# Kernel optimization log

Hardware: AMD Instinct MI355X
Metric: run time of the kernel (lower is better)

## Reference

```python
import jax, jax.numpy as jnp
import numpy as np

D = 1024; H = 16; N = 64; F = 4096
B = 1; T = 2048
W_LORA = 64; A_LORA = 64; V_LORA = 32; G_LORA = 128


def rmsnorm(x, w, eps=1e-6):
    x32 = x.astype(jnp.float32)
    var = jnp.mean(x32 * x32, axis=-1, keepdims=True)
    return w * (x32 * jax.lax.rsqrt(var + eps))


def rwkv7_scan(r, w_log, k, v, a, b, state):
    # r,w_log,k,v,a,b: [B,T,H,N]; state: [B,H,N,N] (value dim, key dim)
    decay = jnp.exp(w_log)  # kernel applies exp to the log-decay w = -exp(w_pre)
    def step(S, inp):
        r_t, d_t, k_t, v_t, a_t, b_t = inp  # each [B,H,N]
        sa = jnp.einsum('bhij,bhj->bhi', S, a_t)
        S = S * d_t[:, :, None, :] + sa[..., None] * b_t[:, :, None, :] + v_t[..., None] * k_t[:, :, None, :]
        o_t = jnp.einsum('bhij,bhj->bhi', S, r_t)
        return S, o_t
    seq = tuple(jnp.moveaxis(t, 1, 0) for t in (r, decay, k, v, a, b))  # [T,B,H,N]
    state_f, o = jax.lax.scan(step, state, seq)
    return jnp.moveaxis(o, 0, 1), state_f  # [B,T,H,N], [B,H,N,N]


def setup_inputs() -> dict:
    key = jax.random.key(0)
    ks = iter(jax.random.split(key, 64))
    def nrm(shape, s=1.0):
        return jax.random.normal(next(ks), shape, dtype=jnp.float32) * s
    def uni(shape):
        return jax.random.uniform(next(ks), shape, dtype=jnp.float32)
    WS = 0.02  # weight scale for big matrices
    inp = {
        'x': nrm((B, T, D)),
        'x_prev': nrm((B, D)),
        'v_first': nrm((B, T, D)),
        'state': jnp.zeros((B, H, N, N), jnp.float32),
        'ln1_w': jnp.ones((D,), jnp.float32),
        'ln2_w': jnp.ones((D,), jnp.float32),
        'x_r': uni((1, 1, D)), 'x_w': uni((1, 1, D)), 'x_k': uni((1, 1, D)),
        'x_v': uni((1, 1, D)), 'x_a': uni((1, 1, D)), 'x_g': uni((1, 1, D)),
        'w0': nrm((1, 1, D), 0.5), 'w1': nrm((D, W_LORA), WS), 'w2': nrm((W_LORA, D), WS),
        'a0': nrm((1, 1, D), 0.1), 'a1': nrm((D, A_LORA), WS), 'a2': nrm((A_LORA, D), WS),
        'v0': nrm((1, 1, D), 0.1), 'v1': nrm((D, V_LORA), WS), 'v2': nrm((V_LORA, D), WS),
        'g1': nrm((D, G_LORA), WS), 'g2': nrm((G_LORA, D), WS),
        'k_k': uni((D,)), 'k_a': uni((D,)), 'r_k': nrm((D,), 0.1),
        'R_': nrm((D, D), WS), 'K_': nrm((D, D), WS), 'V_': nrm((D, D), WS), 'O_': nrm((D, D), WS),
        'gate_w': nrm((D, F), WS), 'up_w': nrm((D, F), WS), 'down_w': nrm((F, D), WS),
    }
    return inp


def _block(x, x_prev, v_first, state, ln1_w, ln2_w, x_r, x_w, x_k, x_v, x_a, x_g,
           w0, w1, w2, a0, a1, a2, v0, v1, v2, g1, g2, k_k, k_a, r_k,
           R_, K_, V_, O_, gate_w, up_w, down_w):
    Bx, Tx, _ = x.shape
    xn = rmsnorm(x, ln1_w)  # ln1
    # token shift
    xx = jnp.concatenate([x_prev[:, None, :], xn[:, :-1]], axis=1) - xn
    xr = xn + xx * x_r; xw = xn + xx * x_w; xk = xn + xx * x_k
    xv = xn + xx * x_v; xa = xn + xx * x_a; xg = xn + xx * x_g
    r = xr @ R_
    w_pre = -jax.nn.softplus(-(w0 + jnp.tanh(xw @ w1) @ w2)) - 0.5
    k = xk @ K_
    v = xv @ V_
    a = jax.nn.sigmoid(a0 + (xa @ a1) @ a2)
    g = jax.nn.sigmoid(xg @ g1) @ g2
    kk = (k * k_k).reshape(Bx, Tx, H, N)
    kk = kk / jnp.maximum(jnp.linalg.norm(kk, axis=-1, keepdims=True), 1e-12)
    kk = kk.reshape(Bx, Tx, H * N)
    k = k * (1 + (a - 1) * k_a)
    # layer_id > 0: lerp toward v_first
    v = v + (v_first - v) * jax.nn.sigmoid(v0 + (xv @ v1) @ v2)
    w_log = -jnp.exp(w_pre)  # log-decay passed to the recurrent kernel
    aa = -kk
    bb = kk * a
    hv = lambda t: t.reshape(Bx, Tx, H, N)
    o, state_f = rwkv7_scan(hv(r), hv(w_log), hv(k), hv(v), hv(aa), hv(bb), state)
    o = o.reshape(Bx, Tx, H * N)
    bonus = ((r * k * r_k).reshape(Bx, Tx, H, N).sum(-1, keepdims=True) * v.reshape(Bx, Tx, H, N)).reshape(Bx, Tx, H * N)
    o = o + bonus
    x = x + (o * g) @ O_
    # SwiGLU MLP
    xm = rmsnorm(x, ln2_w)
    x = x + (jax.nn.silu(xm @ gate_w) * (xm @ up_w)) @ down_w
    return x, xn[:, -1], state_f


def reference(x, x_prev, v_first, state, ln1_w, ln2_w, x_r, x_w, x_k, x_v, x_a, x_g,
              w0, w1, w2, a0, a1, a2, v0, v1, v2, g1, g2, k_k, k_a, r_k,
              R_, K_, V_, O_, gate_w, up_w, down_w):
    return _block(x, x_prev, v_first, state, ln1_w, ln2_w, x_r, x_w, x_k, x_v, x_a, x_g,
                  w0, w1, w2, a0, a1, a2, v0, v1, v2, g1, g2, k_k, k_a, r_k,
                  R_, K_, V_, O_, gate_w, up_w, down_w)
```

## Files before the change

kernel.cpp:

```cpp
#include <hip/hip_runtime.h>
#include <math.h>

#define T_ 2048
#define D_ 1024
#define H_ 16
#define N_ 64
#define F_ 4096
#define NCHUNK 32
#define CLEN 64

typedef __attribute__((ext_vector_type(8))) short bf16x8;
typedef __attribute__((ext_vector_type(4))) float f32x4;
typedef __attribute__((address_space(3))) unsigned int lds_u32_t;
typedef __attribute__((address_space(1))) const unsigned int glb_u32_t;

static __device__ __forceinline__ float sigf(float x) { return 1.0f / (1.0f + __expf(-x)); }

static __device__ __forceinline__ ushort f2bf(float f) {
    union { float f; unsigned u; } c; c.f = f;
    unsigned r = (c.u + 0x7FFFu + ((c.u >> 16) & 1u)) >> 16;
    return (ushort)r;
}
static __device__ __forceinline__ float bf2f(ushort h) {
    union { unsigned u; float f; } c; c.u = ((unsigned)h) << 16;
    return c.f;
}

static __device__ __forceinline__ void st4(float* p, float4 v) { *(float4*)p = v; }
static __device__ __forceinline__ void st4(ushort* p, float4 v) {
    ushort4 o; o.x = f2bf(v.x); o.y = f2bf(v.y); o.z = f2bf(v.z); o.w = f2bf(v.w);
    *(ushort4*)p = o;
}

template <typename OutT>
__global__ __launch_bounds__(256) void rmsnorm_kernel(const float* __restrict__ x,
                                                      const float* __restrict__ w,
                                                      OutT* __restrict__ out,
                                                      float* __restrict__ last) {
    const int t = blockIdx.x;
    const int tid = threadIdx.x;
    const float4* xr = (const float4*)(x + (size_t)t * D_);
    float4 v = xr[tid];
    float ss = v.x * v.x + v.y * v.y + v.z * v.z + v.w * v.w;
    ss += __shfl_xor(ss, 1);
    ss += __shfl_xor(ss, 2);
    ss += __shfl_xor(ss, 4);
    ss += __shfl_xor(ss, 8);
    ss += __shfl_xor(ss, 16);
    ss += __shfl_xor(ss, 32);
    __shared__ float red[4];
    if ((tid & 63) == 0) red[tid >> 6] = ss;
    __syncthreads();
    float tot = red[0] + red[1] + red[2] + red[3];
    float scale = rsqrtf(tot * (1.0f / (float)D_) + 1e-6f);
    float4 wv = ((const float4*)w)[tid];
    float4 o;
    o.x = wv.x * v.x * scale;
    o.y = wv.y * v.y * scale;
    o.z = wv.z * v.z * scale;
    o.w = wv.w * v.w * scale;
    st4(out + (size_t)t * D_ + tid * 4, o);
    if (last != nullptr && t == T_ - 1) ((float4*)last)[tid] = o;
}

__global__ __launch_bounds__(256) void shift_kernel(
    const float* __restrict__ xn, const float* __restrict__ x_prev,
    const float* __restrict__ cr, const float* __restrict__ cw, const float* __restrict__ ck,
    const float* __restrict__ cv, const float* __restrict__ ca, const float* __restrict__ cg,
    ushort* __restrict__ xr, ushort* __restrict__ xw, ushort* __restrict__ xk,
    ushort* __restrict__ xv, ushort* __restrict__ xa, ushort* __restrict__ xg) {
    const int i = blockIdx.x * 256 + threadIdx.x;
    const int t = i >> 8, j = i & 255;
    const float4* xn4 = (const float4*)xn;
    float4 cur = xn4[i];
    float4 prev = (t == 0) ? ((const float4*)x_prev)[j] : xn4[i - 256];
    float4 xx;
    xx.x = prev.x - cur.x;
    xx.y = prev.y - cur.y;
    xx.z = prev.z - cur.z;
    xx.w = prev.w - cur.w;
#define APPLY(dst, c)                                   \
    {                                                   \
        float4 cc = ((const float4*)c)[j];              \
        float4 o;                                       \
        o.x = cur.x + xx.x * cc.x;                      \
        o.y = cur.y + xx.y * cc.y;                      \
        o.z = cur.z + xx.z * cc.z;                      \
        o.w = cur.w + xx.w * cc.w;                      \
        st4(dst + (size_t)i * 4, o);                    \
    }
    APPLY(xr, cr)
    APPLY(xw, cw)
    APPLY(xk, ck)
    APPLY(xv, cv)
    APPLY(xa, ca)
    APPLY(xg, cg)
#undef APPLY
}

struct TDesc { const float* in; ushort* out; int K, N, off; };
struct TPack { TDesc d[15]; };

__global__ __launch_bounds__(256) void transpose_cast_multi(TPack p) {
    __shared__ float tile[32][33];
    const int bid = blockIdx.x;
    int di = 0;
#pragma unroll
    for (int i = 1; i < 15; i++)
        if (bid >= p.d[i].off) di = i;
    const TDesc d = p.d[di];
    const int local = bid - d.off;
    const int nt = d.N >> 5;
    const int bx = local % nt, by = local / nt;
    const int tx = threadIdx.x & 31, ty = threadIdx.x >> 5;
    const int n0 = bx * 32, k0 = by * 32;
#pragma unroll
    for (int i = 0; i < 4; i++)
        tile[ty + i * 8][tx] = d.in[(size_t)(k0 + ty + i * 8) * d.N + n0 + tx];
    __syncthreads();
#pragma unroll
    for (int i = 0; i < 4; i++)
        d.out[(size_t)(n0 + ty + i * 8) * d.K + k0 + tx] = f2bf(tile[tx][ty + i * 8]);
}

template <typename OutT, bool ATOMIC>
__global__ __launch_bounds__(256) void mfma_gemm(
    const ushort* __restrict__ A, const ushort* __restrict__ BT, OutT* __restrict__ C,
    const float* __restrict__ res, const float* __restrict__ res2, const float* __restrict__ bias,
    int M, int Ntot, int K, int klen, int epi) {
    __shared__ ushort As[128 * 32];
    __shared__ ushort Bs[128 * 32];
    const int tid = threadIdx.x;
    const int wave = tid >> 6, lane = tid & 63;
    const int wr = wave >> 1, wc = wave & 1;
    const int lrow = lane & 15, quad = lane >> 4;
    const int m0 = blockIdx.y * 128, n0 = blockIdx.x * 128;
    const int kbase = blockIdx.z * klen;
    const int srow = lane >> 2;
    const int scol = (lane & 3) << 3;

    f32x4 acc[4][4] = {};

    for (int k0 = kbase; k0 < kbase + klen; k0 += 32) {
#pragma unroll
        for (int j = 0; j < 2; j++) {
            const int chunk = 2 * wave + j;
            const ushort* ga = A + (size_t)(m0 + chunk * 16 + srow) * K + k0 + scol;
            __builtin_amdgcn_global_load_lds((glb_u32_t*)ga,
                                             (lds_u32_t*)&As[chunk * 512], 16, 0, 0);
            const int brow = n0 + chunk * 16 + srow;
            const ushort* gb = BT + (size_t)brow * K + k0 + scol;
            if (brow < Ntot)
                __builtin_amdgcn_global_load_lds((glb_u32_t*)gb,
                                                 (lds_u32_t*)&Bs[chunk * 512], 16, 0, 0);
        }
        __syncthreads();
        bf16x8 af[4], bfr[4];
#pragma unroll
        for (int mi = 0; mi < 4; mi++)
            af[mi] = *(const bf16x8*)&As[(wr * 64 + mi * 16 + lrow) * 32 + quad * 8];
#pragma unroll
        for (int ni = 0; ni < 4; ni++)
            bfr[ni] = *(const bf16x8*)&Bs[(wc * 64 + ni * 16 + lrow) * 32 + quad * 8];
#pragma unroll
        for (int mi = 0; mi < 4; mi++)
#pragma unroll
            for (int ni = 0; ni < 4; ni++)
                acc[mi][ni] = __builtin_amdgcn_mfma_f32_16x16x32_bf16(af[mi], bfr[ni], acc[mi][ni], 0, 0, 0);
        __syncthreads();
    }

#pragma unroll
    for (int mi = 0; mi < 4; mi++) {
#pragma unroll
        for (int r = 0; r < 4; r++) {
            const int row = m0 + wr * 64 + mi * 16 + quad * 4 + r;
#pragma unroll
            for (int ni = 0; ni < 4; ni++) {
                const int col = n0 + wc * 64 + ni * 16 + lrow;
                if (col < Ntot) {
                    const size_t idx = (size_t)row * Ntot + col;
                    float val = acc[mi][ni][r];
                    if constexpr (ATOMIC) {
                        atomicAdd((float*)&C[idx], val);
                    } else {
                        switch (epi) {
                            case 1: val += res[idx]; break;
                            case 2: val = val * sigf(val); break;
                            default: break;
                        }
                        if constexpr (sizeof(OutT) == 2) C[idx] = (OutT)f2bf(val);
                        else C[idx] = (OutT)val;
                    }
                }
            }
        }
    }
}

struct MMDesc {
    const ushort* A; const ushort* BT;
    float* Cf; ushort* Cb;
    const float* res; const float* res2; const float* bias;
    int Ntot, K, kbase, klen, epi, atomic;
};
template <int NZ>
struct MMPack { MMDesc d[NZ]; };

template <int NZ>
__global__ __launch_bounds__(256) void mfma_gemm_multi(MMPack<NZ> p) {
    const MMDesc d = p.d[blockIdx.z];
    const int n0 = blockIdx.x * 128;
    if (n0 >= d.Ntot) return;
    __shared__ ushort As[128 * 32];
    __shared__ ushort Bs[128 * 32];
    const int tid = threadIdx.x;
    const int wave = tid >> 6, lane = tid & 63;
    const int wr = wave >> 1, wc = wave & 1;
    const int lrow = lane & 15, quad = lane >> 4;
    const int m0 = blockIdx.y * 128;
    const int srow = lane >> 2;
    const int scol = (lane & 3) << 3;
    const int K = d.K, Ntot = d.Ntot;

    f32x4 acc[4][4] = {};

    for (int k0 = d.kbase; k0 < d.kbase + d.klen; k0 += 32) {
#pragma unroll
        for (int j = 0; j < 2; j++) {
            const int chunk = 2 * wave + j;
            const ushort* ga = d.A + (size_t)(m0 + chunk * 16 + srow) * K + k0 + scol;
            __builtin_amdgcn_global_load_lds((glb_u32_t*)ga,
                                             (lds_u32_t*)&As[chunk * 512], 16, 0, 0);
            const int brow = n0 + chunk * 16 + srow;
            const ushort* gb = d.BT + (size_t)brow * K + k0 + scol;
            if (brow < Ntot)
                __builtin_amdgcn_global_load_lds((glb_u32_t*)gb,
                                                 (lds_u32_t*)&Bs[chunk * 512], 16, 0, 0);
        }
        __syncthreads();
        bf16x8 af[4], bfr[4];
#pragma unroll
        for (int mi = 0; mi < 4; mi++)
            af[mi] = *(const bf16x8*)&As[(wr * 64 + mi * 16 + lrow) * 32 + quad * 8];
#pragma unroll
        for (int ni = 0; ni < 4; ni++)
            bfr[ni] = *(const bf16x8*)&Bs[(wc * 64 + ni * 16 + lrow) * 32 + quad * 8];
#pragma unroll
        for (int mi = 0; mi < 4; mi++)
#pragma unroll
            for (int ni = 0; ni < 4; ni++)
                acc[mi][ni] = __builtin_amdgcn_mfma_f32_16x16x32_bf16(af[mi], bfr[ni], acc[mi][ni], 0, 0, 0);
        __syncthreads();
    }

#pragma unroll
    for (int mi = 0; mi < 4; mi++) {
#pragma unroll
        for (int r = 0; r < 4; r++) {
            const int row = m0 + wr * 64 + mi * 16 + quad * 4 + r;
#pragma unroll
            for (int ni = 0; ni < 4; ni++) {
                const int col = n0 + wc * 64 + ni * 16 + lrow;
                if (col < Ntot) {
                    const size_t idx = (size_t)row * Ntot + col;
                    float val = acc[mi][ni][r];
                    if (d.atomic) {
                        atomicAdd(d.Cf + idx, val);
                    } else {
                        switch (d.epi) {
                            case 3: val = tanhf(val); break;
                            case 4: val = sigf(val); break;
                            case 5: val = sigf(d.bias[col] + val); break;
                            case 6: val = __expf(-0.60653065971263342f * sigf(d.bias[col] + val)); break;
                            case 7: {
                                float vr = d.res[idx];
                                val = vr + (d.res2[idx] - vr) * sigf(d.bias[col] + val);
                            } break;
                            default: break;
                        }
                        if (d.Cb) d.Cb[idx] = f2bf(val);
                        else d.Cf[idx] = val;
                    }
                }
            }
        }
    }
}

__global__ __launch_bounds__(256) void kk_kernel(float* __restrict__ k,
                                                 const float* __restrict__ a_sig,
                                                 const float* __restrict__ k_k,
                                                 const float* __restrict__ k_a,
                                                 float* __restrict__ kk,
                                                 float* __restrict__ mb) {
    const int b = blockIdx.x * 4 + (threadIdx.x >> 6);
    const int t = b >> 4, h = b & 15;
    const int lane = threadIdx.x & 63;
    const size_t idx = (size_t)t * D_ + h * N_ + lane;
    const int wi = h * N_ + lane;
    const float kraw = k[idx];
    const float kv = kraw * k_k[wi];
    float ss = kv * kv;
    ss += __shfl_xor(ss, 1);
    ss += __shfl_xor(ss, 2);
    ss += __shfl_xor(ss, 4);
    ss += __shfl_xor(ss, 8);
    ss += __shfl_xor(ss, 16);
    ss += __shfl_xor(ss, 32);
    const float nrm = fmaxf(sqrtf(ss), 1e-12f);
    const float kkn = kv / nrm;
    kk[idx] = kkn;
    mb[idx] = -kkn * a_sig[idx];
    k[idx] = kraw * (1.0f + (a_sig[idx] - 1.0f) * k_a[wi]);
}

#define FOR16(M) M(0) M(1) M(2) M(3) M(4) M(5) M(6) M(7) \
                 M(8) M(9) M(10) M(11) M(12) M(13) M(14) M(15)

__global__ __launch_bounds__(64, 1) void scan_pass1(
    const float* __restrict__ gR, const float* __restrict__ gD, const float* __restrict__ gK,
    const float* __restrict__ gV, const float* __restrict__ gKK, const float* __restrict__ gMB,
    float* __restrict__ Pbuf, float* __restrict__ Lbuf,
    float* __restrict__ zbuf, float* __restrict__ olbuf) {
    const int bid = blockIdx.x;
    const bool isp = bid >= NCHUNK * H_;
    const int sub = isp ? bid - NCHUNK * H_ : bid;
    const int h = sub & 15;
    const int c = sub >> 4;
    const int lane = threadIdx.x;
    const int hb = h * N_;
    const int t0 = c * CLEN;
    const int tend = t0 + CLEN - 1;

    __shared__ __align__(16) unsigned char ring[2 * 2048];

    const int rsel = lane >> 4;
    const int sub4 = (lane & 15) << 2;
    const float* p1 = (rsel == 0 ? gR : rsel == 1 ? gD : rsel == 2 ? gK : gKK)
                      + (size_t)t0 * D_ + hb + sub4;
    const float* p2 = (rsel == 1 ? gV : gMB) + (size_t)t0 * D_ + hb + sub4;

    const float fid = isp ? 1.0f : 0.0f;
#define DECL(q) f32x4 s##q = {(lane == 4 * q + 0) ? fid : 0.0f, \
                              (lane == 4 * q + 1) ? fid : 0.0f, \
                              (lane == 4 * q + 2) ? fid : 0.0f, \
                              (lane == 4 * q + 3) ? fid : 0.0f};
    FOR16(DECL)
#undef DECL

    float* __restrict__ dotOut = isp ? zbuf : olbuf;

    float4 r0a, r0b, r1a, r1b, r2a, r2b, r3a, r3b;

#define LOADQ(qa, qb, tt) {                                                  \
        const size_t _adv = (size_t)((tt) - t0) * D_;                        \
        qa = *(const float4*)(p1 + _adv);                                    \
        qb = *(const float4*)(p2 + _adv); }
#define WRITEQ(sl, qa, qb) {                                                 \
        *(float4*)(ring + (sl) * 2048 + lane * 16) = qa;                     \
        *(float4*)(ring + (sl) * 2048 + 1024 + lane * 16) = qb; }
#define PA(q) { const f32x4 kk4 = sKKr[q]; sacc += s##q * kk4; }
#define PB(q) {                                                   \
        const f32x4 d4 = sDr[q];                                  \
        const f32x4 k4 = sKr[q];                                  \
        const f32x4 m4 = sMBr[q];                                 \
        const f32x4 r4 = sRr[q];                                  \
        s##q = s##q * d4 + (m4 * sap + k4 * vv);                  \
        oacc += s##q * r4;                                        \
    }
#define COMPUTE(sl, tt) {                                                    \
        const unsigned char* sb = (const unsigned char*)ring + (sl) * 2048;  \
        const f32x4* sRr = (const f32x4*)(sb);                               \
        const f32x4* sDr = (const f32x4*)(sb + 256);                         \
        const f32x4* sKr = (const f32x4*)(sb + 512);                         \
        const f32x4* sKKr = (const f32x4*)(sb + 768);                        \
        const f32x4* sMBr = (const f32x4*)(sb + 1024);                       \
        const float* sVr = (const float*)(sb + 1280);                        \
        f32x4 sacc = {0.f, 0.f, 0.f, 0.f};                                   \
        FOR16(PA)                                                            \
        const float sap = (sacc.x + sacc.y) + (sacc.z + sacc.w);             \
        const float vv = isp ? 0.0f : sVr[lane];                             \
        f32x4 oacc = {0.f, 0.f, 0.f, 0.f};                                   \
        FOR16(PB)                                                            \
        dotOut[(size_t)(tt) * D_ + hb + lane] =                              \
            (oacc.x + oacc.y) + (oacc.z + oacc.w); }

    LOADQ(r0a, r0b, t0)
    LOADQ(r1a, r1b, t0 + 1)
    LOADQ(r2a, r2b, t0 + 2)
    LOADQ(r3a, r3b, t0 + 3)
    WRITEQ(0, r0a, r0b)

    for (int t = t0; t < t0 + CLEN; t += 4) {
        WRITEQ(1, r1a, r1b)
        LOADQ(r0a, r0b, (t + 4 > tend ? tend : t + 4))
        COMPUTE(0, t)
        WRITEQ(0, r2a, r2b)
        LOADQ(r1a, r1b, (t + 5 > tend ? tend : t + 5))
        COMPUTE(1, t + 1)
        WRITEQ(1, r3a, r3b)
        LOADQ(r2a, r2b, (t + 6 > tend ? tend : t + 6))
        COMPUTE(0, t + 2)
        WRITEQ(0, r0a, r0b)
        LOADQ(r3a, r3b, (t + 7 > tend ? tend : t + 7))
        COMPUTE(1, t + 3)
    }
#undef COMPUTE
#undef PB
#undef PA
#undef WRITEQ
#undef LOADQ

    float* __restrict__ sd = isp ? Pbuf : Lbuf;
    const size_t base = ((size_t)c * 16 + h) * 4096 + (size_t)lane * 64;
#define ST(q) *(f32x4*)(sd + base + 4 * q) = s##q;
    FOR16(ST)
#undef ST
}

__global__ __launch_bounds__(256) void scan_combine(
    const float* __restrict__ state_in, const float* __restrict__ Pbuf,
    const float* __restrict__ Lbuf, float* __restrict__ SstT, float* __restrict__ state_out) {
    const int h = blockIdx.x >> 2, rg = blockIdx.x & 3;
    const int tid = threadIdx.x;
    const int i = tid >> 4, j4 = (tid & 15) << 2;
    const int gi = rg * 16 + i;
    __shared__ float Sl[16][68];
    __shared__ float Pl[64][68];

    float4 sv = *(const float4*)(state_in + (size_t)h * 4096 + gi * 64 + j4);
    *(float4*)&Sl[i][j4] = sv;
    __syncthreads();

    for (int c = 0; c < NCHUNK; c++) {
        const size_t cb = ((size_t)c * 16 + h) * 4096;
        float4 scur = *(const float4*)&Sl[i][j4];
        SstT[cb + (size_t)(j4 + 0) * 64 + gi] = scur.x;
        SstT[cb + (size_t)(j4 + 1) * 64 + gi] = scur.y;
        SstT[cb + (size_t)(j4 + 2) * 64 + gi] = scur.z;
        SstT[cb + (size_t)(j4 + 3) * 64 + gi] = scur.w;
#pragma unroll
        for (int q = 0; q < 4; q++) {
            const int pr = (tid >> 4) + q * 16;
            *(float4*)&Pl[pr][j4] = *(const float4*)(Pbuf + cb + (size_t)pr * 64 + j4);
        }
        __syncthreads();
        float4 acc = *(const float4*)(Lbuf + cb + (size_t)gi * 64 + j4);
#pragma unroll 8
        for (int m = 0; m < 64; m++) {
            const float smv = Sl[i][m];
            const float4 p4 = *(const float4*)&Pl[m][j4];
            acc.x = fmaf(smv, p4.x, acc.x);
            acc.y = fmaf(smv, p4.y, acc.y);
            acc.z = fmaf(smv, p4.z, acc.z);
            acc.w = fmaf(smv, p4.w, acc.w);
        }
        __syncthreads();
        *(float4*)&Sl[i][j4] = acc;
        __syncthreads();
    }
    *(float4*)(state_out + (size_t)h * 4096 + gi * 64 + j4) = *(const float4*)&Sl[i][j4];
}

__global__ __launch_bounds__(256) void scan_fix(
    const float* __restrict__ zbuf, const float* __restrict__ olbuf,
    const float* __restrict__ SstT, float* __restrict__ o) {
    const int tg = blockIdx.x >> 4, h = blockIdx.x & 15;
    const int hb = h * N_;
    const int tid = threadIdx.x;
    const int tok = tid >> 4, i4 = (tid & 15) << 2;
    const int tbase = tg * 16;
    const int c = tbase >> 6;
    __shared__ float zl[16][68];
    __shared__ float Sl[64][68];

    *(float4*)&zl[tok][i4] = *(const float4*)(zbuf + (size_t)(tbase + tok) * D_ + hb + i4);
    const size_t cb = ((size_t)c * 16 + h) * 4096;
#pragma unroll
    for (int q = 0; q < 4; q++) {
        const int jr = (tid >> 4) + q * 16;
        *(float4*)&Sl[jr][i4] = *(const float4*)(SstT + cb + (size_t)jr * 64 + i4);
    }
    __syncthreads();
    float4 acc = *(const float4*)(olbuf + (size_t)(tbase + tok) * D_ + hb + i4);
#pragma unroll 8
    for (int j = 0; j < 64; j++) {
        const float zv = zl[tok][j];
        const float4 p4 = *(const float4*)&Sl[j][i4];
        acc.x = fmaf(zv, p4.x, acc.x);
        acc.y = fmaf(zv, p4.y, acc.y);
        acc.z = fmaf(zv, p4.z, acc.z);
        acc.w = fmaf(zv, p4.w, acc.w);
    }
    *(float4*)(o + (size_t)(tbase + tok) * D_ + hb + i4) = acc;
}

__global__ __launch_bounds__(256) void bonus_kernel(const float* __restrict__ o,
                                                    const float* __restrict__ r,
                                                    const float* __restrict__ k,
                                                    const float* __restrict__ v,
                                                    const float* __restrict__ g,
                                                    const float* __restrict__ r_k,
                                                    ushort* __restrict__ og) {
    const int b = blockIdx.x * 4 + (threadIdx.x >> 6);
    const int t = b >> 4, h = b & 15;
    const int lane = threadIdx.x & 63;
    const size_t idx = (size_t)t * D_ + h * N_ + lane;
    float c = r[idx] * k[idx] * r_k[h * N_ + lane];
    c += __shfl_xor(c, 1);
    c += __shfl_xor(c, 2);
    c += __shfl_xor(c, 4);
    c += __shfl_xor(c, 8);
    c += __shfl_xor(c, 16);
    c += __shfl_xor(c, 32);
    const float on = o[idx] + c * v[idx];
    og[idx] = f2bf(on * g[idx]);
}

__global__ __launch_bounds__(256) void mulz_kernel(const ushort* __restrict__ Z,
                                                   ushort* __restrict__ Hb) {
    const int idx = blockIdx.x * 256 + threadIdx.x;
    const int t = idx >> 10;
    const int j = (idx & 1023) << 2;
    const ushort4 zg = *(const ushort4*)(Z + (size_t)t * 8192 + j);
    const ushort4 zu = *(const ushort4*)(Z + (size_t)t * 8192 + 4096 + j);
    ushort4 o;
    float g0 = bf2f(zg.x), g1 = bf2f(zg.y), g2 = bf2f(zg.z), g3 = bf2f(zg.w);
    o.x = f2bf(g0 * sigf(g0) * bf2f(zu.x));
    o.y = f2bf(g1 * sigf(g1) * bf2f(zu.y));
    o.z = f2bf(g2 * sigf(g2) * bf2f(zu.z));
    o.w = f2bf(g3 * sigf(g3) * bf2f(zu.w));
    *(ushort4*)(Hb + (size_t)t * 4096 + j) = o;
}

template <typename OutT, bool ATOMIC = false>
static inline void mm(const ushort* A, const ushort* BT, OutT* C, int M, int Ntot, int K,
                      int nsplit, int epi, const float* res, const float* res2,
                      const float* bias, hipStream_t s) {
    dim3 g((Ntot + 127) / 128, M / 128, nsplit);
    mfma_gemm<OutT, ATOMIC><<<g, 256, 0, s>>>(A, BT, C, res, res2, bias, M, Ntot, K,
                                              K / nsplit, epi);
}

extern "C" void kernel_launch(void* const* d_in, const int* in_sizes, int n_in,
                              void* d_out, int out_size, void* d_ws, size_t ws_size,
                              hipStream_t stream) {
    const float* x      = (const float*)d_in[0];
    const float* x_prev = (const float*)d_in[1];
    const float* v_first= (const float*)d_in[2];
    const float* state  = (const float*)d_in[3];
    const float* ln1_w  = (const float*)d_in[4];
    const float* ln2_w  = (const float*)d_in[5];
    const float* x_r    = (const float*)d_in[6];
    const float* x_w    = (const float*)d_in[7];
    const float* x_k    = (const float*)d_in[8];
    const float* x_v    = (const float*)d_in[9];
    const float* x_a    = (const float*)d_in[10];
    const float* x_g    = (const float*)d_in[11];
    const float* w0     = (const float*)d_in[12];
    const float* w1     = (const float*)d_in[13];
    const float* w2     = (const float*)d_in[14];
    const float* a0     = (const float*)d_in[15];
    const float* a1     = (const float*)d_in[16];
    const float* a2     = (const float*)d_in[17];
    const float* v0     = (const float*)d_in[18];
    const float* v1     = (const float*)d_in[19];
    const float* v2     = (const float*)d_in[20];
    const float* g1     = (const float*)d_in[21];
    const float* g2     = (const float*)d_in[22];
    const float* k_k    = (const float*)d_in[23];
    const float* k_a    = (const float*)d_in[24];
    const float* r_k    = (const float*)d_in[25];
    const float* R_     = (const float*)d_in[26];
    const float* K_     = (const float*)d_in[27];
    const float* V_     = (const float*)d_in[28];
    const float* O_     = (const float*)d_in[29];
    const float* gate_w = (const float*)d_in[30];
    const float* up_w   = (const float*)d_in[31];
    const float* down_w = (const float*)d_in[32];

    float* ws = (float*)d_ws;
    const size_t U = (size_t)T_ * D_;
    float* u_r  = ws;
    float* u_k  = ws + 1 * U;
    float* u_v  = ws + 2 * U;
    float* u_dc = ws + 3 * U;
    float* u_kk = ws + 4 * U;
    float* u_mb = ws + 5 * U;
    float* u_g  = ws + 6 * U;
    float* u_ao = ws + 7 * U;
    ushort* XB = (ushort*)(ws + 8 * U);
    const size_t TD = U;
    ushort* XR = XB + 0 * TD;
    ushort* XW = XB + 1 * TD;
    ushort* XK = XB + 2 * TD;
    ushort* XV = XB + 3 * TD;
    ushort* XA = XB + 4 * TD;
    ushort* XG = XB + 5 * TD;
    ushort* XM   = XB + 0 * TD;
    ushort* OG   = XB + 1 * TD;
    ushort* Hbuf = XB + 2 * TD;
    ushort* Zbuf = (ushort*)ws;
    float* Pbuf  = u_ao;
    float* Lbuf  = (float*)XB;
    float* zbuf  = (float*)(XB + 2 * TD);
    float* olbuf = (float*)(XB + 4 * TD);
    float* SstT  = u_dc;
    float* obuf  = u_kk;
    ushort* WT = (ushort*)(ws + 11 * U);
    const size_t DD = (size_t)D_ * D_;
    const size_t DF = (size_t)D_ * F_;
    ushort* WTR = WT;
    ushort* WTK = WTR + DD;
    ushort* WTV = WTK + DD;
    ushort* WTO = WTV + DD;
    ushort* WTG = WTO + DD;
    ushort* WTU = WTG + DF;
    ushort* WTD = WTU + DF;
    ushort* WTw1 = WTD + DF;
    ushort* WTw2 = WTw1 + 64 * 1024;
    ushort* WTa1 = WTw2 + 64 * 1024;
    ushort* WTa2 = WTa1 + 64 * 1024;
    ushort* WTv1 = WTa2 + 64 * 1024;
    ushort* WTv2 = WTv1 + 32 * 1024;
    ushort* WTg1 = WTv2 + 32 * 1024;
    ushort* WTg2 = WTg1 + 128 * 1024;
    ushort* Lw = WTg2 + 128 * 1024;
    ushort* La = Lw + (size_t)T_ * 64;
    ushort* Lv = La + (size_t)T_ * 64;
    ushort* Lg = Lv + (size_t)T_ * 32;

    float* out_x = (float*)d_out;
    float* out_xn_last = out_x + (size_t)T_ * D_;
    float* out_state = out_xn_last + D_;

    TPack tp;
    int toff = 0, ti = 0;
    auto addT = [&](const float* in, ushort* out, int K, int N) {
        tp.d[ti].in = in; tp.d[ti].out = out; tp.d[ti].K = K; tp.d[ti].N = N; tp.d[ti].off = toff;
        toff += (N / 32) * (K / 32); ++ti;
    };
    addT(R_, WTR, D_, D_);
    addT(K_, WTK, D_, D_);
    addT(V_, WTV, D_, D_);
    addT(O_, WTO, D_, D_);
    addT(gate_w, WTG, D_, F_);
    addT(up_w, WTU, D_, F_);
    addT(down_w, WTD, F_, D_);
    addT(w1, WTw1, D_, 64);
    addT(w2, WTw2, 64, D_);
    addT(a1, WTa1, D_, 64);
    addT(a2, WTa2, 64, D_);
    addT(v1, WTv1, D_, 32);
    addT(v2, WTv2, 32, D_);
    addT(g1, WTg1, D_, 128);
    addT(g2, WTg2, 128, D_);
    transpose_cast_multi<<<toff, 256, 0, stream>>>(tp);

    rmsnorm_kernel<float><<<T_, 256, 0, stream>>>(x, ln1_w, out_x, out_xn_last);
    shift_kernel<<<T_, 256, 0, stream>>>(out_x, x_prev, x_r, x_w, x_k, x_v, x_a, x_g,
                                         XR, XW, XK, XV, XA, XG);
    hipMemsetAsync(u_r, 0, 3 * U * sizeof(float), stream);
    auto mkmm = [](const ushort* A, const ushort* BT, float* Cf, ushort* Cb,
                   const float* res, const float* res2, const float* bias,
                   int Ntot, int K, int kbase, int klen, int epi, int atomic) {
        MMDesc m{A, BT, Cf, Cb, res, res2, bias, Ntot, K, kbase, klen, epi, atomic};
        return m;
    };
    MMPack<10> pa;
    pa.d[0] = mkmm(XR, WTR, u_r, nullptr, nullptr, nullptr, nullptr, D_, D_, 0,   512, 0, 1);
    pa.d[1] = mkmm(XR, WTR, u_r, nullptr, nullptr, nullptr, nullptr, D_, D_, 512, 512, 0, 1);
    pa.d[2] = mkmm(XK, WTK, u_k, nullptr, nullptr, nullptr, nullptr, D_, D_, 0,   512, 0, 1);
    pa.d[3] = mkmm(XK, WTK, u_k, nullptr, nullptr, nullptr, nullptr, D_, D_, 512, 512, 0, 1);
    pa.d[4] = mkmm(XV, WTV, u_v, nullptr, nullptr, nullptr, nullptr, D_, D_, 0,   512, 0, 1);
    pa.d[5] = mkmm(XV, WTV, u_v, nullptr, nullptr, nullptr, nullptr, D_, D_, 512, 512, 0, 1);
    pa.d[6] = mkmm(XW, WTw1, nullptr, Lw, nullptr, nullptr, nullptr, 64,  D_, 0, D_, 3, 0);
    pa.d[7] = mkmm(XA, WTa1, nullptr, La, nullptr, nullptr, nullptr, 64,  D_, 0, D_, 0, 0);
    pa.d[8] = mkmm(XV, WTv1, nullptr, Lv, nullptr, nullptr, nullptr, 32,  D_, 0, D_, 0, 0);
    pa.d[9] = mkmm(XG, WTg1, nullptr, Lg, nullptr, nullptr, nullptr, 128, D_, 0, D_, 4, 0);
    mfma_gemm_multi<10><<<dim3(8, 16, 10), 256, 0, stream>>>(pa);
    MMPack<4> pb;
    pb.d[0] = mkmm(Lw, WTw2, u_dc, nullptr, nullptr, nullptr, w0, D_, 64,  0, 64,  6, 0);
    pb.d[1] = mkmm(La, WTa2, u_ao, nullptr, nullptr, nullptr, a0, D_, 64,  0, 64,  5, 0);
    pb.d[2] = mkmm(Lv, WTv2, u_v,  nullptr, u_v, v_first,     v0, D_, 32,  0, 32,  7, 0);
    pb.d[3] = mkmm(Lg, WTg2, u_g,  nullptr, nullptr, nullptr, nullptr, D_, 128, 0, 128, 0, 0);
    mfma_gemm_multi<4><<<dim3(8, 16, 4), 256, 0, stream>>>(pb);
    kk_kernel<<<T_ * H_ / 4, 256, 0, stream>>>(u_k, u_ao, k_k, k_a, u_kk, u_mb);
    scan_pass1<<<NCHUNK * H_ * 2, 64, 0, stream>>>(u_r, u_dc, u_k, u_v, u_kk, u_mb,
                                                   Pbuf, Lbuf, zbuf, olbuf);
    scan_combine<<<H_ * 4, 256, 0, stream>>>(state, Pbuf, Lbuf, SstT, out_state);
    scan_fix<<<(T_ / 16) * H_, 256, 0, stream>>>(zbuf, olbuf, SstT, obuf);
    bonus_kernel<<<T_ * H_ / 4, 256, 0, stream>>>(obuf, u_r, u_k, u_v, u_g, r_k, OG);
    hipMemcpyAsync(out_x, x, U * sizeof(float), hipMemcpyDeviceToDevice, stream);
    mm<float, true>(OG, WTO, out_x, T_, D_, D_, 2, 0, nullptr, nullptr, nullptr, stream);
    rmsnorm_kernel<ushort><<<T_, 256, 0, stream>>>(out_x, ln2_w, XM, nullptr);
    mm<ushort>(XM, WTG, Zbuf, T_, 2 * F_, D_, 1, 0, nullptr, nullptr, nullptr, stream);
    mulz_kernel<<<(T_ * (F_ / 4)) / 256, 256, 0, stream>>>(Zbuf, Hbuf);
    mm<float, true>(Hbuf, WTD, out_x, T_, D_, F_, 4, 0, nullptr, nullptr, nullptr, stream);
}
```

Measured before the change: 652.6 us.

## Double-buffer GEMM LDS tiles and drop split-K atomics in favor of residual epilogues

Both MFMA GEMM kernels now use two LDS buffers per operand. The next K-slice is prefetched with global_load_lds while the current slice is being multiplied, so only one barrier is needed per iteration. Split-K with atomicAdd is removed everywhere: the R/K/V projections, the output projection and the down projection each run as a single full-K pass, and the residual add moves into the epilogue. That lets the memset and device-to-device memcpy go. The cost is less parallelism: the output and down projections launch only 128 workgroups on a large GPU, and the down projection runs a long K=4096 loop per block, so occupancy can suffer.

```diff
diff --git a/kernel.cpp b/kernel.cpp
--- a/kernel.cpp
+++ b/kernel.cpp
@@ -123,51 +123,57 @@
         d.out[(size_t)(n0 + ty + i * 8) * d.K + k0 + tx] = f2bf(tile[tx][ty + i * 8]);
 }
 
-template <typename OutT, bool ATOMIC>
+template <typename OutT>
 __global__ __launch_bounds__(256) void mfma_gemm(
     const ushort* __restrict__ A, const ushort* __restrict__ BT, OutT* __restrict__ C,
-    const float* __restrict__ res, const float* __restrict__ res2, const float* __restrict__ bias,
-    int M, int Ntot, int K, int klen, int epi) {
-    __shared__ ushort As[128 * 32];
-    __shared__ ushort Bs[128 * 32];
+    const float* res, int M, int Ntot, int K, int epi) {
+    __shared__ ushort As[2][128 * 32];
+    __shared__ ushort Bs[2][128 * 32];
     const int tid = threadIdx.x;
     const int wave = tid >> 6, lane = tid & 63;
     const int wr = wave >> 1, wc = wave & 1;
     const int lrow = lane & 15, quad = lane >> 4;
     const int m0 = blockIdx.y * 128, n0 = blockIdx.x * 128;
-    const int kbase = blockIdx.z * klen;
     const int srow = lane >> 2;
     const int scol = (lane & 3) << 3;
 
     f32x4 acc[4][4] = {};
 
-    for (int k0 = kbase; k0 < kbase + klen; k0 += 32) {
+    auto stage = [&](int buf, int kk) {
 #pragma unroll
         for (int j = 0; j < 2; j++) {
             const int chunk = 2 * wave + j;
-            const ushort* ga = A + (size_t)(m0 + chunk * 16 + srow) * K + k0 + scol;
+            const ushort* ga = A + (size_t)(m0 + chunk * 16 + srow) * K + kk + scol;
             __builtin_amdgcn_global_load_lds((glb_u32_t*)ga,
-                                             (lds_u32_t*)&As[chunk * 512], 16, 0, 0);
+                                             (lds_u32_t*)&As[buf][chunk * 512], 16, 0, 0);
             const int brow = n0 + chunk * 16 + srow;
-            const ushort* gb = BT + (size_t)brow * K + k0 + scol;
-            if (brow < Ntot)
+            if (brow < Ntot) {
+                const ushort* gb = BT + (size_t)brow * K + kk + scol;
                 __builtin_amdgcn_global_load_lds((glb_u32_t*)gb,
-                                                 (lds_u32_t*)&Bs[chunk * 512], 16, 0, 0);
+                                                 (lds_u32_t*)&Bs[buf][chunk * 512], 16, 0, 0);
+            }
         }
-        __syncthreads();
+    };
+
+    stage(0, 0);
+    __syncthreads();
+    int cur = 0;
+    for (int k0 = 0; k0 < K; k0 += 32) {
+        if (k0 + 32 < K) stage(cur ^ 1, k0 + 32);
         bf16x8 af[4], bfr[4];
 #pragma unroll
         for (int mi = 0; mi < 4; mi++)
-            af[mi] = *(const bf16x8*)&As[(wr * 64 + mi * 16 + lrow) * 32 + quad * 8];
+            af[mi] = *(const bf16x8*)&As[cur][(wr * 64 + mi * 16 + lrow) * 32 + quad * 8];
 #pragma unroll
         for (int ni = 0; ni < 4; ni++)
-            bfr[ni] = *(const bf16x8*)&Bs[(wc * 64 + ni * 16 + lrow) * 32 + quad * 8];
+            bfr[ni] = *(const bf16x8*)&Bs[cur][(wc * 64 + ni * 16 + lrow) * 32 + quad * 8];
 #pragma unroll
         for (int mi = 0; mi < 4; mi++)
 #pragma unroll
             for (int ni = 0; ni < 4; ni++)
                 acc[mi][ni] = __builtin_amdgcn_mfma_f32_16x16x32_bf16(af[mi], bfr[ni], acc[mi][ni], 0, 0, 0);
         __syncthreads();
+        cur ^= 1;
     }
 
 #pragma unroll
@@ -181,17 +187,9 @@
                 if (col < Ntot) {
                     const size_t idx = (size_t)row * Ntot + col;
                     float val = acc[mi][ni][r];
-                    if constexpr (ATOMIC) {
-                        atomicAdd((float*)&C[idx], val);
-                    } else {
-                        switch (epi) {
-                            case 1: val += res[idx]; break;
-                            case 2: val = val * sigf(val); break;
-                            default: break;
-                        }
-                        if constexpr (sizeof(OutT) == 2) C[idx] = (OutT)f2bf(val);
-                        else C[idx] = (OutT)val;
-                    }
+                    if (epi == 1) val += res[idx];
+                    if constexpr (sizeof(OutT) == 2) C[idx] = (OutT)f2bf(val);
+                    else C[idx] = (OutT)val;
                 }
             }
         }
@@ -202,7 +200,7 @@
     const ushort* A; const ushort* BT;
     float* Cf; ushort* Cb;
     const float* res; const float* res2; const float* bias;
-    int Ntot, K, kbase, klen, epi, atomic;
+    int Ntot, K, epi;
 };
 template <int NZ>
 struct MMPack { MMDesc d[NZ]; };
@@ -212,8 +210,8 @@
     const MMDesc d = p.d[blockIdx.z];
     const int n0 = blockIdx.x * 128;
     if (n0 >= d.Ntot) return;
-    __shared__ ushort As[128 * 32];
-    __shared__ ushort Bs[128 * 32];
+    __shared__ ushort As[2][128 * 32];
+    __shared__ ushort Bs[2][128 * 32];
     const int tid = threadIdx.x;
     const int wave = tid >> 6, lane = tid & 63;
     const int wr = wave >> 1, wc = wave & 1;
@@ -225,33 +223,41 @@
 
     f32x4 acc[4][4] = {};
 
-    for (int k0 = d.kbase; k0 < d.kbase + d.klen; k0 += 32) {
+    auto stage = [&](int buf, int kk) {
 #pragma unroll
         for (int j = 0; j < 2; j++) {
             const int chunk = 2 * wave + j;
-            const ushort* ga = d.A + (size_t)(m0 + chunk * 16 + srow) * K + k0 + scol;
+            const ushort* ga = d.A + (size_t)(m0 + chunk * 16 + srow) * K + kk + scol;
             __builtin_amdgcn_global_load_lds((glb_u32_t*)ga,
-                                             (lds_u32_t*)&As[chunk * 512], 16, 0, 0);
+                                             (lds_u32_t*)&As[buf][chunk * 512], 16, 0, 0);
             const int brow = n0 + chunk * 16 + srow;
-            const ushort* gb = d.BT + (size_t)brow * K + k0 + scol;
-            if (brow < Ntot)
+            if (brow < Ntot) {
+                const ushort* gb = d.BT + (size_t)brow * K + kk + scol;
                 __builtin_amdgcn_global_load_lds((glb_u32_t*)gb,
-                                                 (lds_u32_t*)&Bs[chunk * 512], 16, 0, 0);
+                                                 (lds_u32_t*)&Bs[buf][chunk * 512], 16, 0, 0);
+            }
         }
-        __syncthreads();
+    };
+
+    stage(0, 0);
+    __syncthreads();
+    int cur = 0;
+    for (int k0 = 0; k0 < K; k0 += 32) {
+        if (k0 + 32 < K) stage(cur ^ 1, k0 + 32);
         bf16x8 af[4], bfr[4];
 #pragma unroll
         for (int mi = 0; mi < 4; mi++)
-            af[mi] = *(const bf16x8*)&As[(wr * 64 + mi * 16 + lrow) * 32 + quad * 8];
+            af[mi] = *(const bf16x8*)&As[cur][(wr * 64 + mi * 16 + lrow) * 32 + quad * 8];
 #pragma unroll
         for (int ni = 0; ni < 4; ni++)
-            bfr[ni] = *(const bf16x8*)&Bs[(wc * 64 + ni * 16 + lrow) * 32 + quad * 8];
+            bfr[ni] = *(const bf16x8*)&Bs[cur][(wc * 64 + ni * 16 + lrow) * 32 + quad * 8];
 #pragma unroll
         for (int mi = 0; mi < 4; mi++)
 #pragma unroll
             for (int ni = 0; ni < 4; ni++)
                 acc[mi][ni] = __builtin_amdgcn_mfma_f32_16x16x32_bf16(af[mi], bfr[ni], acc[mi][ni], 0, 0, 0);
         __syncthreads();
+        cur ^= 1;
     }
 
 #pragma unroll
@@ -265,23 +271,19 @@
                 if (col < Ntot) {
                     const size_t idx = (size_t)row * Ntot + col;
                     float val = acc[mi][ni][r];
-                    if (d.atomic) {
-                        atomicAdd(d.Cf + idx, val);
-                    } else {
-                        switch (d.epi) {
-                            case 3: val = tanhf(val); break;
-                            case 4: val = sigf(val); break;
-                            case 5: val = sigf(d.bias[col] + val); break;
-                            case 6: val = __expf(-0.60653065971263342f * sigf(d.bias[col] + val)); break;
-                            case 7: {
-                                float vr = d.res[idx];
-                                val = vr + (d.res2[idx] - vr) * sigf(d.bias[col] + val);
-                            } break;
-                            default: break;
-                        }
-                        if (d.Cb) d.Cb[idx] = f2bf(val);
-                        else d.Cf[idx] = val;
+                    switch (d.epi) {
+                        case 3: val = tanhf(val); break;
+                        case 4: val = sigf(val); break;
+                        case 5: val = sigf(d.bias[col] + val); break;
+                        case 6: val = __expf(-0.60653065971263342f * sigf(d.bias[col] + val)); break;
+                        case 7: {
+                            float vr = d.res[idx];
+                            val = vr + (d.res2[idx] - vr) * sigf(d.bias[col] + val);
+                        } break;
+                        default: break;
                     }
+                    if (d.Cb) d.Cb[idx] = f2bf(val);
+                    else d.Cf[idx] = val;
                 }
             }
         }
@@ -532,15 +534,6 @@
     o.z = f2bf(g2 * sigf(g2) * bf2f(zu.z));
     o.w = f2bf(g3 * sigf(g3) * bf2f(zu.w));
     *(ushort4*)(Hb + (size_t)t * 4096 + j) = o;
-}
-
-template <typename OutT, bool ATOMIC = false>
-static inline void mm(const ushort* A, const ushort* BT, OutT* C, int M, int Ntot, int K,
-                      int nsplit, int epi, const float* res, const float* res2,
-                      const float* bias, hipStream_t s) {
-    dim3 g((Ntot + 127) / 128, M / 128, nsplit);
-    mfma_gemm<OutT, ATOMIC><<<g, 256, 0, s>>>(A, BT, C, res, res2, bias, M, Ntot, K,
-                                              K / nsplit, epi);
 }
 
 extern "C" void kernel_launch(void* const* d_in, const int* in_sizes, int n_in,
@@ -661,30 +654,26 @@
     rmsnorm_kernel<float><<<T_, 256, 0, stream>>>(x, ln1_w, out_x, out_xn_last);
     shift_kernel<<<T_, 256, 0, stream>>>(out_x, x_prev, x_r, x_w, x_k, x_v, x_a, x_g,
                                          XR, XW, XK, XV, XA, XG);
-    hipMemsetAsync(u_r, 0, 3 * U * sizeof(float), stream);
     auto mkmm = [](const ushort* A, const ushort* BT, float* Cf, ushort* Cb,
                    const float* res, const float* res2, const float* bias,
-                   int Ntot, int K, int kbase, int klen, int epi, int atomic) {
-        MMDesc m{A, BT, Cf, Cb, res, res2, bias, Ntot, K, kbase, klen, epi, atomic};
+                   int Ntot, int K, int epi) {
+        MMDesc m{A, BT, Cf, Cb, res, res2, bias, Ntot, K, epi};
         return m;
     };
-    MMPack<10> pa;
-    pa.d[0] = mkmm(XR, WTR, u_r, nullptr, nullptr, nullptr, nullptr, D_, D_, 0,   512, 0, 1);
-    pa.d[1] = mkmm(XR, WTR, u_r, nullptr, nullptr, nullptr, nullptr, D_, D_, 512, 512, 0, 1);
-    pa.d[2] = mkmm(XK, WTK, u_k, nullptr, nullptr, nullptr, nullptr, D_, D_, 0,   512, 0, 1);
-    pa.d[3] = mkmm(XK, WTK, u_k, nullptr, nullptr, nullptr, nullptr, D_, D_, 512, 512, 0, 1);
-    pa.d[4] = mkmm(XV, WTV, u_v, nullptr, nullptr, nullptr, nullptr, D_, D_, 0,   512, 0, 1);
-    pa.d[5] = mkmm(XV, WTV, u_v, nullptr, nullptr, nullptr, nullptr, D_, D_, 512, 512, 0, 1);
-    pa.d[6] = mkmm(XW, WTw1, nullptr, Lw, nullptr, nullptr, nullptr, 64,  D_, 0, D_, 3, 0);
-    pa.d[7] = mkmm(XA, WTa1, nullptr, La, nullptr, nullptr, nullptr, 64,  D_, 0, D_, 0, 0);
-    pa.d[8] = mkmm(XV, WTv1, nullptr, Lv, nullptr, nullptr, nullptr, 32,  D_, 0, D_, 0, 0);
-    pa.d[9] = mkmm(XG, WTg1, nullptr, Lg, nullptr, nullptr, nullptr, 128, D_, 0, D_, 4, 0);
-    mfma_gemm_multi<10><<<dim3(8, 16, 10), 256, 0, stream>>>(pa);
+    MMPack<7> pa;
+    pa.d[0] = mkmm(XR, WTR, u_r, nullptr, nullptr, nullptr, nullptr, D_, D_, 0);
+    pa.d[1] = mkmm(XK, WTK, u_k, nullptr, nullptr, nullptr, nullptr, D_, D_, 0);
+    pa.d[2] = mkmm(XV, WTV, u_v, nullptr, nullptr, nullptr, nullptr, D_, D_, 0);
+    pa.d[3] = mkmm(XW, WTw1, nullptr, Lw, nullptr, nullptr, nullptr, 64,  D_, 3);
+    pa.d[4] = mkmm(XA, WTa1, nullptr, La, nullptr, nullptr, nullptr, 64,  D_, 0);
+    pa.d[5] = mkmm(XV, WTv1, nullptr, Lv, nullptr, nullptr, nullptr, 32,  D_, 0);
+    pa.d[6] = mkmm(XG, WTg1, nullptr, Lg, nullptr, nullptr, nullptr, 128, D_, 4);
+    mfma_gemm_multi<7><<<dim3(8, 16, 7), 256, 0, stream>>>(pa);
     MMPack<4> pb;
-    pb.d[0] = mkmm(Lw, WTw2, u_dc, nullptr, nullptr, nullptr, w0, D_, 64,  0, 64,  6, 0);
-    pb.d[1] = mkmm(La, WTa2, u_ao, nullptr, nullptr, nullptr, a0, D_, 64,  0, 64,  5, 0);
-    pb.d[2] = mkmm(Lv, WTv2, u_v,  nullptr, u_v, v_first,     v0, D_, 32,  0, 32,  7, 0);
-    pb.d[3] = mkmm(Lg, WTg2, u_g,  nullptr, nullptr, nullptr, nullptr, D_, 128, 0, 128, 0, 0);
+    pb.d[0] = mkmm(Lw, WTw2, u_dc, nullptr, nullptr, nullptr, w0, D_, 64,  6);
+    pb.d[1] = mkmm(La, WTa2, u_ao, nullptr, nullptr, nullptr, a0, D_, 64,  5);
+    pb.d[2] = mkmm(Lv, WTv2, u_v,  nullptr, u_v, v_first,     v0, D_, 32,  7);
+    pb.d[3] = mkmm(Lg, WTg2, u_g,  nullptr, nullptr, nullptr, nullptr, D_, 128, 0);
     mfma_gemm_multi<4><<<dim3(8, 16, 4), 256, 0, stream>>>(pb);
     kk_kernel<<<T_ * H_ / 4, 256, 0, stream>>>(u_k, u_ao, k_k, k_a, u_kk, u_mb);
     scan_pass1<<<NCHUNK * H_ * 2, 64, 0, stream>>>(u_r, u_dc, u_k, u_v, u_kk, u_mb,
@@ -692,10 +681,9 @@
     scan_combine<<<H_ * 4, 256, 0, stream>>>(state, Pbuf, Lbuf, SstT, out_state);
     scan_fix<<<(T_ / 16) * H_, 256, 0, stream>>>(zbuf, olbuf, SstT, obuf);
     bonus_kernel<<<T_ * H_ / 4, 256, 0, stream>>>(obuf, u_r, u_k, u_v, u_g, r_k, OG);
-    hipMemcpyAsync(out_x, x, U * sizeof(float), hipMemcpyDeviceToDevice, stream);
-    mm<float, true>(OG, WTO, out_x, T_, D_, D_, 2, 0, nullptr, nullptr, nullptr, stream);
+    mfma_gemm<float><<<dim3(8, 16), 256, 0, stream>>>(OG, WTO, out_x, x, T_, D_, D_, 1);
     rmsnorm_kernel<ushort><<<T_, 256, 0, stream>>>(out_x, ln2_w, XM, nullptr);
-    mm<ushort>(XM, WTG, Zbuf, T_, 2 * F_, D_, 1, 0, nullptr, nullptr, nullptr, stream);
+    mfma_gemm<ushort><<<dim3(64, 16), 256, 0, stream>>>(XM, WTG, Zbuf, nullptr, T_, 2 * F_, D_, 0);
     mulz_kernel<<<(T_ * (F_ / 4)) / 256, 256, 0, stream>>>(Zbuf, Hbuf);
-    mm<float, true>(Hbuf, WTD, out_x, T_, D_, F_, 4, 0, nullptr, nullptr, nullptr, stream);
-}
+    mfma_gemm<float><<<dim3(8, 16), 256, 0, stream>>>(Hbuf, WTD, out_x, out_x, T_, D_, F_, 1);
+}
```

After: 661.4 us. Within noise of the previous version (+1.3%).
